# Optimization experiments

Hardware: AMD Instinct MI355X
Metric: run time of the kernel (lower is better)

Reference implementation:

```python
import jax, jax.numpy as jnp
import numpy as np

NUM_HEADS = 8
HEAD_DIM = 128
ATTN_SCALE = 0.12


def _rope_tables(T, head_dim, dtype=jnp.float32):
    # half-truncate RoPE from modded-nanogpt: base-freq bounded, half the dims unrotated
    angular_freq = (1.0 / 1024.0) ** jnp.linspace(0.0, 1.0, head_dim // 4, dtype=dtype)
    angular_freq = jnp.concatenate([angular_freq, jnp.zeros(head_dim // 4, dtype=dtype)])  # [D/2]
    t = jnp.arange(T, dtype=dtype)
    theta = t[:, None] * angular_freq[None, :]  # [T, D/2]
    return jnp.cos(theta), jnp.sin(theta)


def _apply_rope(x, cos, sin):
    # x: [B, T, H, D]; cos/sin: [T, D/2]
    x1, x2 = jnp.split(x, 2, axis=-1)
    c = cos[None, :, None, :]
    s = sin[None, :, None, :]
    y1 = x1 * c + x2 * s
    y2 = x2 * c - x1 * s
    return jnp.concatenate([y1, y2], axis=-1)


def _rms_norm(x):
    eps = jnp.asarray(jnp.finfo(x.dtype).eps, x.dtype)
    var = jnp.mean(jnp.square(x), axis=-1, keepdims=True)
    return x * jax.lax.rsqrt(var + eps)


def setup_inputs() -> dict:
    key = jax.random.key(0)
    ks = jax.random.split(key, 4)
    B, T, dim = 1, 4096, 1024
    hdim = NUM_HEADS * HEAD_DIM
    std = 0.5 * dim ** (-0.5)
    bound = (3.0 ** 0.5) * std
    x = jax.random.normal(ks[0], (B, T, dim), dtype=jnp.float32)
    ve = jax.random.normal(ks[1], (B, T, hdim), dtype=jnp.float32)
    qkv_w = jax.random.uniform(ks[2], (3, hdim, dim), dtype=jnp.float32, minval=-bound, maxval=bound)
    lambdas = jnp.array([0.5, 0.5], dtype=jnp.float32)
    c_proj_w = jax.random.normal(ks[3], (dim, hdim), dtype=jnp.float32) * 0.02
    return {"x": x, "ve": ve, "qkv_w": qkv_w, "lambdas": lambdas, "c_proj_w": c_proj_w}


def reference(x, ve, qkv_w, lambdas, c_proj_w):
    B, T, dim = x.shape
    H, D = NUM_HEADS, HEAD_DIM
    # fused QKV projection: qkv_w is [3, H*D, dim]
    w = qkv_w.reshape(3 * H * D, dim)
    qkv = jnp.einsum('btd,fd->btf', x, w).reshape(B, T, 3, H, D)
    q, k, v = qkv[:, :, 0], qkv[:, :, 1], qkv[:, :, 2]  # each [B, T, H, D]
    q = _rms_norm(q)
    k = _rms_norm(k)
    cos, sin = _rope_tables(T, D, dtype=jnp.float32)
    q = _apply_rope(q, cos, sin)
    k = _apply_rope(k, cos, sin)
    # lambda-weighted value blend with value embeddings
    v = lambdas[0] * v + lambdas[1] * ve.reshape(B, T, H, D)
    # causal attention, scale = 0.12
    scores = jnp.einsum('bthd,bshd->bhts', q, k) * ATTN_SCALE  # [B, H, T, T]
    causal = jnp.tril(jnp.ones((T, T), dtype=bool))
    scores = jnp.where(causal[None, None, :, :], scores, jnp.asarray(-jnp.inf, scores.dtype))
    p = jax.nn.softmax(scores, axis=-1)
    y = jnp.einsum('bhts,bshd->bthd', p, v).reshape(B, T, H * D)
    return jnp.einsum('btf,df->btd', y, c_proj_w)
```

## Files before the change

kernel.cpp:

```cpp
#include <hip/hip_runtime.h>
#include <hip/hip_bf16.h>

typedef __attribute__((ext_vector_type(4))) float f32x4;
typedef __attribute__((ext_vector_type(16))) float f32x16;
typedef __attribute__((ext_vector_type(8))) __bf16 bf16x8;
typedef unsigned short u16;
typedef unsigned int u32;
typedef __attribute__((ext_vector_type(4))) u16 u16x4;

__device__ __forceinline__ u16 f2bf(float f) {
    u32 u = __builtin_bit_cast(u32, f);
    u32 r = (u + 0x7FFFu + ((u >> 16) & 1u)) >> 16;
    return (u16)r;
}
__device__ __forceinline__ float bf2f(u16 h) {
    return __builtin_bit_cast(float, ((u32)h) << 16);
}
__device__ __forceinline__ bf16x8 ld_frag(const u16* p) {
    uint4 v = *reinterpret_cast<const uint4*>(p);
    return __builtin_bit_cast(bf16x8, v);
}
__device__ __forceinline__ void gld_lds(const u16* gp, u16* lp) {
    __builtin_amdgcn_global_load_lds(
        (const __attribute__((address_space(1))) u32*)gp,
        (__attribute__((address_space(3))) u32*)lp, 16, 0, 0);
}
__device__ __forceinline__ u32 pk_bf16(float lo, float hi) {
    u32 r;
    asm("v_cvt_pk_bf16_f32 %0, %1, %2" : "=v"(r) : "v"(lo), "v"(hi));
    return r;
}
__device__ __forceinline__ void unp8(uint4 v, float* f) {
    f[0] = bf2f((u16)(v.x & 0xffffu)); f[1] = bf2f((u16)(v.x >> 16));
    f[2] = bf2f((u16)(v.y & 0xffffu)); f[3] = bf2f((u16)(v.y >> 16));
    f[4] = bf2f((u16)(v.z & 0xffffu)); f[5] = bf2f((u16)(v.z >> 16));
    f[6] = bf2f((u16)(v.w & 0xffffu)); f[7] = bf2f((u16)(v.w >> 16));
}

__global__ __launch_bounds__(256) void cvt3(const float* __restrict__ x,
                                            const float* __restrict__ w,
                                            const float* __restrict__ c,
                                            u16* __restrict__ xb,
                                            u16* __restrict__ wb,
                                            u16* __restrict__ cb) {
    int b = blockIdx.x;
    const float* in;
    u16* out;
    int i;
    if (b < 4096)      { in = x; out = xb; i = b * 256 + threadIdx.x; }
    else if (b < 7168) { in = w; out = wb; i = (b - 4096) * 256 + threadIdx.x; }
    else               { in = c; out = cb; i = (b - 7168) * 256 + threadIdx.x; }
    float4 v = reinterpret_cast<const float4*>(in)[i];
    u16x4 o;
    o.x = f2bf(v.x); o.y = f2bf(v.y); o.z = f2bf(v.z); o.w = f2bf(v.w);
    *reinterpret_cast<u16x4*>(out + 4 * (size_t)i) = o;
}

__global__ __launch_bounds__(256) void rope_tab(float* __restrict__ ctab,
                                                float* __restrict__ stab) {
    int i = blockIdx.x * 256 + threadIdx.x;
    int t = i >> 6, j = i & 63;
    float c = 1.0f, s = 0.0f;
    if (j < 32) {
        float f = exp2f(-10.0f * (float)j / 31.0f);
        float th = (float)t * f;
        c = cosf(th); s = sinf(th);
    }
    ctab[i] = c; stab[i] = s;
}

template <bool OUT_BF16>
__global__ __launch_bounds__(256) void gemm_nt(const u16* __restrict__ A,
                                               const u16* __restrict__ B,
                                               void* __restrict__ Cout,
                                               int M, int N, int K, int ldc) {
    __shared__ u16 sA[2][128 * 32];
    __shared__ u16 sB[2][128 * 32];
    const int tid = threadIdx.x;
    const int w = tid >> 6, l = tid & 63;
    const int mb = M >> 7;
    const int bm = blockIdx.x % mb, bn = blockIdx.x / mb;
    const int g = l >> 4, c16 = l & 15;
    const int srow = l >> 2, ssl = l & 3;
    const int wr = w >> 1, wc = w & 1;

    f32x4 acc[4][4] = {};

    auto stage = [&](int bi, int kt) {
#pragma unroll
        for (int cc = 0; cc < 2; ++cc) {
            int c = 2 * w + cc;
            int r = 16 * c + srow;
            int gs = ssl ^ ((r >> 1) & 3);
            gld_lds(A + (size_t)(bm * 128 + r) * K + kt * 32 + gs * 8, &sA[bi][c * 512]);
            gld_lds(B + (size_t)(bn * 128 + r) * K + kt * 32 + gs * 8, &sB[bi][c * 512]);
        }
    };

    const int NT = K >> 5;
    stage(0, 0);
    __syncthreads();
    for (int kt = 0; kt < NT; ++kt) {
        int cur = kt & 1;
        if (kt + 1 < NT) stage(cur ^ 1, kt + 1);
        bf16x8 af[4], bf[4];
#pragma unroll
        for (int mi = 0; mi < 4; ++mi) {
            int r = wr * 64 + mi * 16 + c16;
            int sl = g ^ ((r >> 1) & 3);
            af[mi] = ld_frag(&sA[cur][r * 32 + sl * 8]);
        }
#pragma unroll
        for (int ni = 0; ni < 4; ++ni) {
            int r = wc * 64 + ni * 16 + c16;
            int sl = g ^ ((r >> 1) & 3);
            bf[ni] = ld_frag(&sB[cur][r * 32 + sl * 8]);
        }
#pragma unroll
        for (int mi = 0; mi < 4; ++mi)
#pragma unroll
            for (int ni = 0; ni < 4; ++ni)
                acc[mi][ni] = __builtin_amdgcn_mfma_f32_16x16x32_bf16(
                    af[mi], bf[ni], acc[mi][ni], 0, 0, 0);
        __syncthreads();
    }
#pragma unroll
    for (int mi = 0; mi < 4; ++mi) {
#pragma unroll
        for (int ni = 0; ni < 4; ++ni) {
            int col = bn * 128 + wc * 64 + ni * 16 + c16;
            int row0 = bm * 128 + wr * 64 + mi * 16 + g * 4;
#pragma unroll
            for (int r = 0; r < 4; ++r) {
                if (OUT_BF16)
                    ((u16*)Cout)[(size_t)(row0 + r) * ldc + col] = f2bf(acc[mi][ni][r]);
                else
                    ((float*)Cout)[(size_t)(row0 + r) * ldc + col] = acc[mi][ni][r];
            }
        }
    }
}

__global__ __launch_bounds__(256) void prep(const u16* __restrict__ qkvb,
                                            const float* __restrict__ ve,
                                            const float* __restrict__ lambdas,
                                            const float* __restrict__ ctab,
                                            const float* __restrict__ stab,
                                            u16* __restrict__ Qb, u16* __restrict__ Kb,
                                            u16* __restrict__ Vt) {
    __shared__ u16 sV[128 * 72];
    const int h = blockIdx.x >> 6, tb = blockIdx.x & 63;
    const int tid = threadIdx.x;
    const int trow = tid >> 2, p = tid & 3;
    const int t = tb * 64 + trow;
    const float l0 = lambdas[0], l1 = lambdas[1];
    const int cperm = (trow & 51) | ((trow & 4) << 1) | ((trow & 8) >> 1);

#pragma unroll
    for (int which = 0; which < 2; ++which) {
        const u16* src = qkvb + (size_t)t * 3072 + which * 1024 + h * 128;
        int j0 = p * 16;
        float x1[16], x2[16];
        unp8(*(const uint4*)(src + j0), x1);
        unp8(*(const uint4*)(src + j0 + 8), x1 + 8);
        unp8(*(const uint4*)(src + 64 + j0), x2);
        unp8(*(const uint4*)(src + 64 + j0 + 8), x2 + 8);
        float ss = 0.0f;
#pragma unroll
        for (int e = 0; e < 16; ++e) ss += x1[e] * x1[e] + x2[e] * x2[e];
        ss += __shfl_xor(ss, 1);
        ss += __shfl_xor(ss, 2);
        float rs = rsqrtf(ss * (1.0f / 128.0f) + 1.1920929e-07f);
        float scl = which ? 1.0f : 0.12f;
        rs *= scl;
        u16* dst = (which ? Kb : Qb) + ((size_t)h * 4096 + t) * 128;
#pragma unroll
        for (int e = 0; e < 16; ++e) {
            int j = j0 + e;
            float c = ctab[t * 64 + j], s = stab[t * 64 + j];
            float a = x1[e] * rs, b = x2[e] * rs;
            dst[j] = f2bf(a * c + b * s);
            dst[j + 64] = f2bf(b * c - a * s);
        }
    }
    {
        const u16* vsrc = qkvb + (size_t)t * 3072 + 2048 + h * 128 + p * 32;
        const float* vesrc = ve + (size_t)t * 1024 + h * 128 + p * 32;
#pragma unroll
        for (int q8 = 0; q8 < 4; ++q8) {
            float vf[8];
            unp8(*(const uint4*)(vsrc + q8 * 8), vf);
            float4 e0 = *(const float4*)(vesrc + q8 * 8);
            float4 e1 = *(const float4*)(vesrc + q8 * 8 + 4);
            float ee[8] = {e0.x, e0.y, e0.z, e0.w, e1.x, e1.y, e1.z, e1.w};
#pragma unroll
            for (int j = 0; j < 8; ++j) {
                float vv = l0 * vf[j] + l1 * ee[j];
                sV[(p * 32 + q8 * 8 + j) * 72 + cperm] = f2bf(vv);
            }
        }
    }
    __syncthreads();
    {
        int d = tid >> 1, seg = tid & 1;
        const u16* lsrc = &sV[d * 72 + seg * 32];
        u16* gdst = Vt + ((size_t)h * 128 + d) * 4096 + tb * 64 + seg * 32;
#pragma unroll
        for (int q2 = 0; q2 < 4; ++q2)
            *(uint4*)(gdst + q2 * 8) = *(const uint4*)(lsrc + q2 * 8);
    }
}

#define OPHALF 4194304
__global__ __launch_bounds__(256) void attn(const u16* __restrict__ Qb,
                                            const u16* __restrict__ Kb,
                                            const u16* __restrict__ Vt,
                                            float* __restrict__ Op,
                                            float* __restrict__ ssumP) {
    __shared__ u16 smem[3 * 8192];
    const int bid = blockIdx.x;
    const int h = bid & 7;
    const int pid = bid >> 3;
    const int j = pid >> 1;
    const int half = pid & 1;
    const int tid = threadIdx.x;
    const int w = tid >> 6, l = tid & 63;
    const int qh = w & 1, kvh = w >> 1;
    const int l31 = l & 31, hi = l >> 5;
    const int krow = kvh * 32 + l31;

    for (int seg = 0; seg < 2; ++seg) {
        const int qb = seg ? (63 - j) : j;
        const int part = seg ? (1 - half) : half;
        const int s = (qb + 1) >> 1;
        const int t0 = part ? s : 0;
        const int t1 = part ? (qb + 1) : s;
        const int qg = qb * 64 + qh * 32 + l31;

        bf16x8 qf[8];
        {
            const u16* qp = Qb + ((size_t)h * 4096 + qg) * 128;
#pragma unroll
            for (int dk = 0; dk < 8; ++dk) qf[dk] = ld_frag(qp + dk * 16 + hi * 8);
        }

        const u16* kp[4];
        const u16* vp[4];
#pragma unroll
        for (int cc = 0; cc < 4; ++cc) {
            int c = 4 * w + cc;
            int rK = 4 * c + (l >> 4);
            int gsK = (l & 15) ^ (rK & 7);
            kp[cc] = Kb + ((size_t)h * 4096 + t0 * 64 + rK) * 128 + gsK * 8;
            int rV = 8 * c + (l >> 3);
            int gsV = (l & 7) ^ (rV & 7);
            vp[cc] = Vt + ((size_t)h * 128 + rV) * 4096 + t0 * 64 + gsV * 8;
        }

        f32x16 o[4] = {};
        float ssum = 0.0f;

        if (t0 < t1) {
#pragma unroll
            for (int cc = 0; cc < 4; ++cc) {
                gld_lds(kp[cc], smem + (4 * w + cc) * 512);
                kp[cc] += 8192;
            }
            __syncthreads();

            int cur = 0;
            for (int t = t0; t < t1; ++t) {
                if (t + 1 < t1) {
#pragma unroll
                    for (int cc = 0; cc < 4; ++cc) {
                        gld_lds(kp[cc], smem + (cur ^ 1) * 8192 + (4 * w + cc) * 512);
                        kp[cc] += 8192;
                    }
                }
#pragma unroll
                for (int cc = 0; cc < 4; ++cc) {
                    gld_lds(vp[cc], smem + 16384 + (4 * w + cc) * 512);
                    vp[cc] += 64;
                }

                const u16* sKc = smem + cur * 8192;
                f32x16 st = {};
                __builtin_amdgcn_s_setprio(1);
#pragma unroll
                for (int dk = 0; dk < 8; ++dk) {
                    int sl = (2 * dk + hi) ^ (krow & 7);
                    bf16x8 kf = ld_frag(sKc + krow * 128 + sl * 8);
                    st = __builtin_amdgcn_mfma_f32_32x32x16_bf16(kf, qf[dk], st, 0, 0, 0);
                }
                __builtin_amdgcn_s_setprio(0);

                float pv[16];
                if (t == qb) {
#pragma unroll
                    for (int r = 0; r < 16; ++r) {
                        int kvg = t * 64 + kvh * 32 + (r & 3) + 8 * (r >> 2) + 4 * hi;
                        pv[r] = (kvg <= qg) ? __expf(st[r]) : 0.0f;
                    }
                } else {
#pragma unroll
                    for (int r = 0; r < 16; ++r) pv[r] = __expf(st[r]);
                }
                float ps = 0.0f;
#pragma unroll
                for (int i = 0; i < 16; ++i) ps += pv[i];
                ssum += ps;

                bf16x8 pb[2];
#pragma unroll
                for (int m = 0; m < 2; ++m) {
                    uint4 u;
                    u.x = pk_bf16(pv[8 * m + 0], pv[8 * m + 1]);
                    u.y = pk_bf16(pv[8 * m + 2], pv[8 * m + 3]);
                    u.z = pk_bf16(pv[8 * m + 4], pv[8 * m + 5]);
                    u.w = pk_bf16(pv[8 * m + 6], pv[8 * m + 7]);
                    pb[m] = __builtin_bit_cast(bf16x8, u);
                }

                __syncthreads();

                const u16* sVc = smem + 16384;
                __builtin_amdgcn_s_setprio(1);
#pragma unroll
                for (int m = 0; m < 2; ++m) {
#pragma unroll
                    for (int dt = 0; dt < 4; ++dt) {
                        int drow = dt * 32 + l31;
                        int sl = (4 * kvh + 2 * m + hi) ^ (drow & 7);
                        bf16x8 vf = ld_frag(sVc + drow * 64 + sl * 8);
                        o[dt] = __builtin_amdgcn_mfma_f32_32x32x16_bf16(vf, pb[m], o[dt], 0, 0, 0);
                    }
                }
                __builtin_amdgcn_s_setprio(0);
                __syncthreads();
                cur ^= 1;
            }
        } else {
            __syncthreads();
        }

        ssum += __shfl_xor(ssum, 32);

        float* sO = (float*)smem;
        float* sS = (float*)smem + 8448;
        if (kvh == 1) {
            float* base = sO + (qh * 32 + l31) * 132;
#pragma unroll
            for (int dt = 0; dt < 4; ++dt)
#pragma unroll
                for (int i = 0; i < 4; ++i) {
                    int d0 = dt * 32 + i * 8 + hi * 4;
                    float4 v = {o[dt][4 * i + 0], o[dt][4 * i + 1],
                                o[dt][4 * i + 2], o[dt][4 * i + 3]};
                    *(float4*)(base + d0) = v;
                }
            if (hi == 0) sS[qh * 32 + l31] = ssum;
        }
        __syncthreads();
        if (kvh == 0) {
            float stot = ssum + sS[qh * 32 + l31];
            const float* base = sO + (qh * 32 + l31) * 132;
            float* orow = Op + (size_t)part * OPHALF + ((size_t)(h * 4096 + qg)) * 128;
#pragma unroll
            for (int dt = 0; dt < 4; ++dt)
#pragma unroll
                for (int i = 0; i < 4; ++i) {
                    int d0 = dt * 32 + i * 8 + hi * 4;
                    float4 prev = *(const float4*)(base + d0);
                    float4 ov = {o[dt][4 * i + 0] + prev.x, o[dt][4 * i + 1] + prev.y,
                                 o[dt][4 * i + 2] + prev.z, o[dt][4 * i + 3] + prev.w};
                    *(float4*)(orow + d0) = ov;
                }
            if (hi == 0) ssumP[part * 32768 + h * 4096 + qg] = stot;
        }
        __syncthreads();
    }
}

__global__ __launch_bounds__(256) void combine(const float* __restrict__ Op,
                                               const float* __restrict__ ssumP,
                                               u16* __restrict__ Y) {
    int i = blockIdx.x * 256 + threadIdx.x;
    int d4 = i & 31;
    int hq = i >> 5;
    int h = hq >> 12, q = hq & 4095;
    float4 a = ((const float4*)Op)[i];
    float4 b = ((const float4*)(Op + OPHALF))[i];
    float inv = 1.0f / (ssumP[hq] + ssumP[32768 + hq]);
    u16x4 ov;
    ov.x = f2bf((a.x + b.x) * inv);
    ov.y = f2bf((a.y + b.y) * inv);
    ov.z = f2bf((a.z + b.z) * inv);
    ov.w = f2bf((a.w + b.w) * inv);
    *(u16x4*)(Y + (size_t)q * 1024 + h * 128 + d4 * 4) = ov;
}

extern "C" void kernel_launch(void* const* d_in, const int* in_sizes, int n_in,
                              void* d_out, int out_size, void* d_ws, size_t ws_size,
                              hipStream_t stream) {
    const float* x = (const float*)d_in[0];
    const float* ve = (const float*)d_in[1];
    const float* qkv_w = (const float*)d_in[2];
    const float* lambdas = (const float*)d_in[3];
    const float* c_proj_w = (const float*)d_in[4];

    char* ws = (char*)d_ws;
    size_t o = 0;
    u16* qkvb = (u16*)(ws + o); o += (size_t)4096 * 3072 * 2;
    u16* xb   = (u16*)(ws + o); o += (size_t)4096 * 1024 * 2;
    u16* wb   = (u16*)(ws + o); o += (size_t)3072 * 1024 * 2;
    u16* cb   = (u16*)(ws + o); o += (size_t)1024 * 1024 * 2;
    u16* Qb   = (u16*)(ws + o); o += (size_t)8 * 4096 * 128 * 2;
    u16* Kb   = (u16*)(ws + o); o += (size_t)8 * 4096 * 128 * 2;
    u16* Vt   = (u16*)(ws + o); o += (size_t)8 * 4096 * 128 * 2;
    u16* Yb   = (u16*)(ws + o); o += (size_t)4096 * 1024 * 2;
    float* ctab = (float*)(ws + o); o += (size_t)4096 * 64 * 4;
    float* stab = (float*)(ws + o); o += (size_t)4096 * 64 * 4;
    float* Op    = (float*)qkvb;
    float* ssumP = (float*)wb;

    cvt3<<<8192, 256, 0, stream>>>(x, qkv_w, c_proj_w, xb, wb, cb);
    rope_tab<<<1024, 256, 0, stream>>>(ctab, stab);
    gemm_nt<true><<<32 * 24, 256, 0, stream>>>(xb, wb, qkvb, 4096, 3072, 1024, 3072);
    prep<<<512, 256, 0, stream>>>(qkvb, ve, lambdas, ctab, stab, Qb, Kb, Vt);
    attn<<<512, 256, 0, stream>>>(Qb, Kb, Vt, Op, ssumP);
    combine<<<4096, 256, 0, stream>>>(Op, ssumP, Yb);
    gemm_nt<false><<<32 * 8, 256, 0, stream>>>(Yb, cb, d_out, 4096, 1024, 1024, 1024);
}
```

Baseline: 147.3 us.

## Split attention KV range three ways with bf16 partials and exp2 softmax

The attention kernel now splits each query block's KV range into three parts instead of two, launching 768 blocks instead of 512 so more work is in flight across CUs. Partial outputs are stored as bf16 rather than fp32 to shrink combine traffic, and combine sums three partials. The log2(e) factor is folded into the Q scale so exp2f replaces __expf. The costs are an extra partial write and read, bf16 rounding of unnormalized partial sums, and uneven split sizes for short query blocks.

Measured after the change: 167.2 us. 1.13x slower.

```diff
diff --git a/kernel.cpp b/kernel.cpp
--- a/kernel.cpp
+++ b/kernel.cpp
@@ -171,7 +171,7 @@
         ss += __shfl_xor(ss, 1);
         ss += __shfl_xor(ss, 2);
         float rs = rsqrtf(ss * (1.0f / 128.0f) + 1.1920929e-07f);
-        float scl = which ? 1.0f : 0.12f;
+        float scl = which ? 1.0f : 0.12f * 1.44269504f;
         rs *= scl;
         u16* dst = (which ? Kb : Qb) + ((size_t)h * 4096 + t) * 128;
 #pragma unroll
@@ -211,18 +211,18 @@
     }
 }
 
-#define OPHALF 4194304
+#define OPPART 4194304
 __global__ __launch_bounds__(256) void attn(const u16* __restrict__ Qb,
                                             const u16* __restrict__ Kb,
                                             const u16* __restrict__ Vt,
-                                            float* __restrict__ Op,
+                                            u16* __restrict__ Op,
                                             float* __restrict__ ssumP) {
     __shared__ u16 smem[3 * 8192];
     const int bid = blockIdx.x;
     const int h = bid & 7;
     const int pid = bid >> 3;
-    const int j = pid >> 1;
-    const int half = pid & 1;
+    const int j = pid / 3;
+    const int p0 = pid % 3;
     const int tid = threadIdx.x;
     const int w = tid >> 6, l = tid & 63;
     const int qh = w & 1, kvh = w >> 1;
@@ -231,10 +231,10 @@
 
     for (int seg = 0; seg < 2; ++seg) {
         const int qb = seg ? (63 - j) : j;
-        const int part = seg ? (1 - half) : half;
-        const int s = (qb + 1) >> 1;
-        const int t0 = part ? s : 0;
-        const int t1 = part ? (qb + 1) : s;
+        const int part = seg ? (2 - p0) : p0;
+        const int ntt = qb + 1;
+        const int t0 = part * ntt / 3;
+        const int t1 = (part + 1) * ntt / 3;
         const int qg = qb * 64 + qh * 32 + l31;
 
         bf16x8 qf[8];
@@ -299,11 +299,11 @@
 #pragma unroll
                     for (int r = 0; r < 16; ++r) {
                         int kvg = t * 64 + kvh * 32 + (r & 3) + 8 * (r >> 2) + 4 * hi;
-                        pv[r] = (kvg <= qg) ? __expf(st[r]) : 0.0f;
+                        pv[r] = (kvg <= qg) ? exp2f(st[r]) : 0.0f;
                     }
                 } else {
 #pragma unroll
-                    for (int r = 0; r < 16; ++r) pv[r] = __expf(st[r]);
+                    for (int r = 0; r < 16; ++r) pv[r] = exp2f(st[r]);
                 }
                 float ps = 0.0f;
 #pragma unroll
@@ -364,16 +364,19 @@
         if (kvh == 0) {
             float stot = ssum + sS[qh * 32 + l31];
             const float* base = sO + (qh * 32 + l31) * 132;
-            float* orow = Op + (size_t)part * OPHALF + ((size_t)(h * 4096 + qg)) * 128;
+            u16* orow = Op + (size_t)part * OPPART + ((size_t)(h * 4096 + qg)) * 128;
 #pragma unroll
             for (int dt = 0; dt < 4; ++dt)
 #pragma unroll
                 for (int i = 0; i < 4; ++i) {
                     int d0 = dt * 32 + i * 8 + hi * 4;
                     float4 prev = *(const float4*)(base + d0);
-                    float4 ov = {o[dt][4 * i + 0] + prev.x, o[dt][4 * i + 1] + prev.y,
-                                 o[dt][4 * i + 2] + prev.z, o[dt][4 * i + 3] + prev.w};
-                    *(float4*)(orow + d0) = ov;
+                    u16x4 ov;
+                    ov.x = f2bf(o[dt][4 * i + 0] + prev.x);
+                    ov.y = f2bf(o[dt][4 * i + 1] + prev.y);
+                    ov.z = f2bf(o[dt][4 * i + 2] + prev.z);
+                    ov.w = f2bf(o[dt][4 * i + 3] + prev.w);
+                    *(u16x4*)(orow + d0) = ov;
                 }
             if (hi == 0) ssumP[part * 32768 + h * 4096 + qg] = stot;
         }
@@ -381,21 +384,22 @@
     }
 }
 
-__global__ __launch_bounds__(256) void combine(const float* __restrict__ Op,
+__global__ __launch_bounds__(256) void combine(const u16* __restrict__ Op,
                                                const float* __restrict__ ssumP,
                                                u16* __restrict__ Y) {
     int i = blockIdx.x * 256 + threadIdx.x;
     int d4 = i & 31;
     int hq = i >> 5;
     int h = hq >> 12, q = hq & 4095;
-    float4 a = ((const float4*)Op)[i];
-    float4 b = ((const float4*)(Op + OPHALF))[i];
-    float inv = 1.0f / (ssumP[hq] + ssumP[32768 + hq]);
+    u16x4 a = ((const u16x4*)Op)[i];
+    u16x4 b = ((const u16x4*)(Op + OPPART))[i];
+    u16x4 c = ((const u16x4*)(Op + 2 * OPPART))[i];
+    float inv = 1.0f / (ssumP[hq] + ssumP[32768 + hq] + ssumP[65536 + hq]);
     u16x4 ov;
-    ov.x = f2bf((a.x + b.x) * inv);
-    ov.y = f2bf((a.y + b.y) * inv);
-    ov.z = f2bf((a.z + b.z) * inv);
-    ov.w = f2bf((a.w + b.w) * inv);
+    ov.x = f2bf((bf2f(a.x) + bf2f(b.x) + bf2f(c.x)) * inv);
+    ov.y = f2bf((bf2f(a.y) + bf2f(b.y) + bf2f(c.y)) * inv);
+    ov.z = f2bf((bf2f(a.z) + bf2f(b.z) + bf2f(c.z)) * inv);
+    ov.w = f2bf((bf2f(a.w) + bf2f(b.w) + bf2f(c.w)) * inv);
     *(u16x4*)(Y + (size_t)q * 1024 + h * 128 + d4 * 4) = ov;
 }
 
@@ -420,14 +424,14 @@
     u16* Yb   = (u16*)(ws + o); o += (size_t)4096 * 1024 * 2;
     float* ctab = (float*)(ws + o); o += (size_t)4096 * 64 * 4;
     float* stab = (float*)(ws + o); o += (size_t)4096 * 64 * 4;
-    float* Op    = (float*)qkvb;
-    float* ssumP = (float*)wb;
+    u16* Op      = qkvb;
+    float* ssumP = (float*)xb;
 
     cvt3<<<8192, 256, 0, stream>>>(x, qkv_w, c_proj_w, xb, wb, cb);
     rope_tab<<<1024, 256, 0, stream>>>(ctab, stab);
     gemm_nt<true><<<32 * 24, 256, 0, stream>>>(xb, wb, qkvb, 4096, 3072, 1024, 3072);
     prep<<<512, 256, 0, stream>>>(qkvb, ve, lambdas, ctab, stab, Qb, Kb, Vt);
-    attn<<<512, 256, 0, stream>>>(Qb, Kb, Vt, Op, ssumP);
+    attn<<<768, 256, 0, stream>>>(Qb, Kb, Vt, Op, ssumP);
     combine<<<4096, 256, 0, stream>>>(Op, ssumP, Yb);
     gemm_nt<false><<<32 * 8, 256, 0, stream>>>(Yb, cb, d_out, 4096, 1024, 1024, 1024);
 }
```

## Fuse RMS norm, RoPE and value blend into the QKV GEMM epilogue

Applied to the files above, without the earlier changes.

The separate prep kernel is removed, and its work moves into the epilogue of a specialized QKV GEMM. Each 128x128 output tile maps to a single head of Q, K or V. The tile is staged through shared memory to do the RMS norm and RoPE, or the lambda blend with ve plus the transposed V write. This drops the bf16 qkv intermediate round trip through global memory and one kernel launch. The cost is a heavier epilogue and more shared memory per block, which may reduce occupancy.

New measurement: 153.6 us. 4.3% more time.

```diff
diff --git a/kernel.cpp b/kernel.cpp
--- a/kernel.cpp
+++ b/kernel.cpp
@@ -69,11 +69,143 @@
     ctab[i] = c; stab[i] = s;
 }
 
-template <bool OUT_BF16>
-__global__ __launch_bounds__(256) void gemm_nt(const u16* __restrict__ A,
-                                               const u16* __restrict__ B,
-                                               void* __restrict__ Cout,
-                                               int M, int N, int K, int ldc) {
+__global__ __launch_bounds__(256) void gemm_qkv(const u16* __restrict__ A,
+                                                const u16* __restrict__ B,
+                                                const float* __restrict__ ve,
+                                                const float* __restrict__ lambdas,
+                                                const float* __restrict__ ctab,
+                                                const float* __restrict__ stab,
+                                                u16* __restrict__ Qb,
+                                                u16* __restrict__ Kb,
+                                                u16* __restrict__ Vt) {
+    __shared__ u16 smem[17408];
+    const int K = 1024;
+    const int tid = threadIdx.x;
+    const int w = tid >> 6, l = tid & 63;
+    const int bm = blockIdx.x & 31, bn = blockIdx.x >> 5;
+    const int g = l >> 4, c16 = l & 15;
+    const int srow = l >> 2, ssl = l & 3;
+    const int wr = w >> 1, wc = w & 1;
+
+    f32x4 acc[4][4] = {};
+
+    auto stage = [&](int bi, int kt) {
+#pragma unroll
+        for (int cc = 0; cc < 2; ++cc) {
+            int c = 2 * w + cc;
+            int r = 16 * c + srow;
+            int gs = ssl ^ ((r >> 1) & 3);
+            gld_lds(A + (size_t)(bm * 128 + r) * K + kt * 32 + gs * 8,
+                    smem + bi * 4096 + c * 512);
+            gld_lds(B + (size_t)(bn * 128 + r) * K + kt * 32 + gs * 8,
+                    smem + 8192 + bi * 4096 + c * 512);
+        }
+    };
+
+    const int NT = K >> 5;
+    stage(0, 0);
+    __syncthreads();
+    for (int kt = 0; kt < NT; ++kt) {
+        int cur = kt & 1;
+        if (kt + 1 < NT) stage(cur ^ 1, kt + 1);
+        bf16x8 af[4], bf[4];
+#pragma unroll
+        for (int mi = 0; mi < 4; ++mi) {
+            int r = wr * 64 + mi * 16 + c16;
+            int sl = g ^ ((r >> 1) & 3);
+            af[mi] = ld_frag(smem + cur * 4096 + r * 32 + sl * 8);
+        }
+#pragma unroll
+        for (int ni = 0; ni < 4; ++ni) {
+            int r = wc * 64 + ni * 16 + c16;
+            int sl = g ^ ((r >> 1) & 3);
+            bf[ni] = ld_frag(smem + 8192 + cur * 4096 + r * 32 + sl * 8);
+        }
+#pragma unroll
+        for (int mi = 0; mi < 4; ++mi)
+#pragma unroll
+            for (int ni = 0; ni < 4; ++ni)
+                acc[mi][ni] = __builtin_amdgcn_mfma_f32_16x16x32_bf16(
+                    af[mi], bf[ni], acc[mi][ni], 0, 0, 0);
+        __syncthreads();
+    }
+
+    const int which = bn >> 3, h = bn & 7;
+    if (which < 2) {
+#pragma unroll
+        for (int mi = 0; mi < 4; ++mi)
+#pragma unroll
+            for (int ni = 0; ni < 4; ++ni) {
+                int col = wc * 64 + ni * 16 + c16;
+                int row0 = wr * 64 + mi * 16 + g * 4;
+#pragma unroll
+                for (int r = 0; r < 4; ++r)
+                    smem[(row0 + r) * 136 + col] = f2bf(acc[mi][ni][r]);
+            }
+        __syncthreads();
+        const int row = tid >> 1, p = tid & 1;
+        const int t = bm * 128 + row;
+        const u16* src = smem + row * 136;
+        const int j0 = p * 32;
+        float x1[32], x2[32];
+#pragma unroll
+        for (int e = 0; e < 32; e += 8) {
+            unp8(*(const uint4*)(src + j0 + e), x1 + e);
+            unp8(*(const uint4*)(src + 64 + j0 + e), x2 + e);
+        }
+        float ss = 0.0f;
+#pragma unroll
+        for (int e = 0; e < 32; ++e) ss += x1[e] * x1[e] + x2[e] * x2[e];
+        ss += __shfl_xor(ss, 1);
+        float rs = rsqrtf(ss * (1.0f / 128.0f) + 1.1920929e-07f);
+        if (which == 0) rs *= 0.12f;
+        u16* dst = (which ? Kb : Qb) + ((size_t)h * 4096 + t) * 128;
+        u16 o1[32], o2[32];
+#pragma unroll
+        for (int e = 0; e < 32; ++e) {
+            int j = j0 + e;
+            float c = ctab[t * 64 + j], s = stab[t * 64 + j];
+            float a = x1[e] * rs, b = x2[e] * rs;
+            o1[e] = f2bf(a * c + b * s);
+            o2[e] = f2bf(b * c - a * s);
+        }
+#pragma unroll
+        for (int e = 0; e < 32; e += 4) {
+            *(u16x4*)(dst + j0 + e) = *(u16x4*)(o1 + e);
+            *(u16x4*)(dst + 64 + j0 + e) = *(u16x4*)(o2 + e);
+        }
+    } else {
+        const float l0 = lambdas[0], l1 = lambdas[1];
+#pragma unroll
+        for (int mi = 0; mi < 4; ++mi)
+#pragma unroll
+            for (int ni = 0; ni < 4; ++ni) {
+                int col = wc * 64 + ni * 16 + c16;
+                int row0 = wr * 64 + mi * 16 + g * 4;
+#pragma unroll
+                for (int r = 0; r < 4; ++r) {
+                    int row = row0 + r;
+                    float vv = l0 * acc[mi][ni][r]
+                             + l1 * ve[(size_t)(bm * 128 + row) * 1024 + h * 128 + col];
+                    int u = row & 63, seg = row >> 6;
+                    int cp = (u & 51) | ((u & 4) << 1) | ((u & 8) >> 1);
+                    smem[col * 136 + seg * 64 + cp] = f2bf(vv);
+                }
+            }
+        __syncthreads();
+        const int d = tid >> 1, seg = tid & 1;
+        const u16* lsrc = smem + d * 136 + seg * 64;
+        u16* gdst = Vt + ((size_t)h * 128 + d) * 4096 + bm * 128 + seg * 64;
+#pragma unroll
+        for (int q2 = 0; q2 < 8; ++q2)
+            *(uint4*)(gdst + q2 * 8) = *(const uint4*)(lsrc + q2 * 8);
+    }
+}
+
+__global__ __launch_bounds__(256) void gemm_nt_f32(const u16* __restrict__ A,
+                                                   const u16* __restrict__ B,
+                                                   float* __restrict__ Cout,
+                                                   int M, int N, int K, int ldc) {
     __shared__ u16 sA[2][128 * 32];
     __shared__ u16 sB[2][128 * 32];
     const int tid = threadIdx.x;
@@ -131,83 +263,9 @@
             int col = bn * 128 + wc * 64 + ni * 16 + c16;
             int row0 = bm * 128 + wr * 64 + mi * 16 + g * 4;
 #pragma unroll
-            for (int r = 0; r < 4; ++r) {
-                if (OUT_BF16)
-                    ((u16*)Cout)[(size_t)(row0 + r) * ldc + col] = f2bf(acc[mi][ni][r]);
-                else
-                    ((float*)Cout)[(size_t)(row0 + r) * ldc + col] = acc[mi][ni][r];
-            }
-        }
-    }
-}
-
-__global__ __launch_bounds__(256) void prep(const u16* __restrict__ qkvb,
-                                            const float* __restrict__ ve,
-                                            const float* __restrict__ lambdas,
-                                            const float* __restrict__ ctab,
-                                            const float* __restrict__ stab,
-                                            u16* __restrict__ Qb, u16* __restrict__ Kb,
-                                            u16* __restrict__ Vt) {
-    __shared__ u16 sV[128 * 72];
-    const int h = blockIdx.x >> 6, tb = blockIdx.x & 63;
-    const int tid = threadIdx.x;
-    const int trow = tid >> 2, p = tid & 3;
-    const int t = tb * 64 + trow;
-    const float l0 = lambdas[0], l1 = lambdas[1];
-    const int cperm = (trow & 51) | ((trow & 4) << 1) | ((trow & 8) >> 1);
-
-#pragma unroll
-    for (int which = 0; which < 2; ++which) {
-        const u16* src = qkvb + (size_t)t * 3072 + which * 1024 + h * 128;
-        int j0 = p * 16;
-        float x1[16], x2[16];
-        unp8(*(const uint4*)(src + j0), x1);
-        unp8(*(const uint4*)(src + j0 + 8), x1 + 8);
-        unp8(*(const uint4*)(src + 64 + j0), x2);
-        unp8(*(const uint4*)(src + 64 + j0 + 8), x2 + 8);
-        float ss = 0.0f;
-#pragma unroll
-        for (int e = 0; e < 16; ++e) ss += x1[e] * x1[e] + x2[e] * x2[e];
-        ss += __shfl_xor(ss, 1);
-        ss += __shfl_xor(ss, 2);
-        float rs = rsqrtf(ss * (1.0f / 128.0f) + 1.1920929e-07f);
-        float scl = which ? 1.0f : 0.12f;
-        rs *= scl;
-        u16* dst = (which ? Kb : Qb) + ((size_t)h * 4096 + t) * 128;
-#pragma unroll
-        for (int e = 0; e < 16; ++e) {
-            int j = j0 + e;
-            float c = ctab[t * 64 + j], s = stab[t * 64 + j];
-            float a = x1[e] * rs, b = x2[e] * rs;
-            dst[j] = f2bf(a * c + b * s);
-            dst[j + 64] = f2bf(b * c - a * s);
-        }
-    }
-    {
-        const u16* vsrc = qkvb + (size_t)t * 3072 + 2048 + h * 128 + p * 32;
-        const float* vesrc = ve + (size_t)t * 1024 + h * 128 + p * 32;
-#pragma unroll
-        for (int q8 = 0; q8 < 4; ++q8) {
-            float vf[8];
-            unp8(*(const uint4*)(vsrc + q8 * 8), vf);
-            float4 e0 = *(const float4*)(vesrc + q8 * 8);
-            float4 e1 = *(const float4*)(vesrc + q8 * 8 + 4);
-            float ee[8] = {e0.x, e0.y, e0.z, e0.w, e1.x, e1.y, e1.z, e1.w};
-#pragma unroll
-            for (int j = 0; j < 8; ++j) {
-                float vv = l0 * vf[j] + l1 * ee[j];
-                sV[(p * 32 + q8 * 8 + j) * 72 + cperm] = f2bf(vv);
-            }
-        }
-    }
-    __syncthreads();
-    {
-        int d = tid >> 1, seg = tid & 1;
-        const u16* lsrc = &sV[d * 72 + seg * 32];
-        u16* gdst = Vt + ((size_t)h * 128 + d) * 4096 + tb * 64 + seg * 32;
-#pragma unroll
-        for (int q2 = 0; q2 < 4; ++q2)
-            *(uint4*)(gdst + q2 * 8) = *(const uint4*)(lsrc + q2 * 8);
+            for (int r = 0; r < 4; ++r)
+                Cout[(size_t)(row0 + r) * ldc + col] = acc[mi][ni][r];
+        }
     }
 }
 
@@ -425,9 +483,8 @@
 
     cvt3<<<8192, 256, 0, stream>>>(x, qkv_w, c_proj_w, xb, wb, cb);
     rope_tab<<<1024, 256, 0, stream>>>(ctab, stab);
-    gemm_nt<true><<<32 * 24, 256, 0, stream>>>(xb, wb, qkvb, 4096, 3072, 1024, 3072);
-    prep<<<512, 256, 0, stream>>>(qkvb, ve, lambdas, ctab, stab, Qb, Kb, Vt);
+    gemm_qkv<<<32 * 24, 256, 0, stream>>>(xb, wb, ve, lambdas, ctab, stab, Qb, Kb, Vt);
     attn<<<512, 256, 0, stream>>>(Qb, Kb, Vt, Op, ssumP);
     combine<<<4096, 256, 0, stream>>>(Op, ssumP, Yb);
-    gemm_nt<false><<<32 * 8, 256, 0, stream>>>(Yb, cb, d_out, 4096, 1024, 1024, 1024);
-}
+    gemm_nt_f32<<<32 * 8, 256, 0, stream>>>(Yb, cb, (float*)d_out, 4096, 1024, 1024, 1024);
+}
```
